# Kernel tuning notes

Hardware: AMD Instinct MI355X
Metric: run time of the kernel (lower is better)

## Reference

```python
import jax, jax.numpy as jnp
import numpy as np

D = 768
H = 12
HD = D // H
EPS = 1e-5

def layer_norm(x, g, b):
    xf = x.astype(jnp.float32)
    mu = jnp.mean(xf, axis=-1, keepdims=True)
    var = jnp.var(xf, axis=-1, keepdims=True)
    return ((xf - mu) * jax.lax.rsqrt(var + EPS) * g + b).astype(x.dtype)

def quick_gelu(x):
    return x * jax.nn.sigmoid(1.702 * x)

def setup_inputs() -> dict:
    key = jax.random.key(0)
    ks = jax.random.split(key, 8)
    L, N = 257, 64
    s = 1.0 / np.sqrt(D)
    return {
        "x": jax.random.normal(ks[0], (L, N, D), dtype=jnp.float32),
        "in_proj_w": jax.random.normal(ks[1], (3 * D, D), dtype=jnp.float32) * s,
        "in_proj_b": jnp.zeros((3 * D,), dtype=jnp.float32),
        "out_proj_w": jax.random.normal(ks[2], (D, D), dtype=jnp.float32) * s,
        "out_proj_b": jnp.zeros((D,), dtype=jnp.float32),
        "ln1_g": jnp.ones((D,), dtype=jnp.float32),
        "ln1_b": jnp.zeros((D,), dtype=jnp.float32),
        "ln2_g": jnp.ones((D,), dtype=jnp.float32),
        "ln2_b": jnp.zeros((D,), dtype=jnp.float32),
        "fc_w": jax.random.normal(ks[3], (D, D), dtype=jnp.float32) * s,
        "fc_b": jnp.zeros((D,), dtype=jnp.float32),
    }

def reference(x, in_proj_w, in_proj_b, out_proj_w, out_proj_b,
              ln1_g, ln1_b, ln2_g, ln2_b, fc_w, fc_b):
    L, N, _ = x.shape
    h = layer_norm(x, ln1_g, ln1_b)                      # [L,N,D]
    qkv = h @ in_proj_w.T + in_proj_b                    # [L,N,3D]
    q, k, v = jnp.split(qkv, 3, axis=-1)
    q = q.reshape(L, N, H, HD)
    k = k.reshape(L, N, H, HD)
    v = v.reshape(L, N, H, HD)
    scale = 1.0 / np.sqrt(HD)
    scores = jnp.einsum('lnhd,mnhd->nhlm', q, k) * scale  # [N,H,L,L]
    weights = jax.nn.softmax(scores, axis=-1)             # per-head attn weights
    attn = jnp.einsum('nhlm,mnhd->lnhd', weights, v).reshape(L, N, D)
    attn_out = attn @ out_proj_w.T + out_proj_b
    x = x + attn_out
    h2 = layer_norm(x, ln2_g, ln2_b)
    x = x + quick_gelu(h2 @ fc_w.T + fc_b)
    return x, weights
```

## Files before the change

### kernel.cpp

```cpp
#include <hip/hip_runtime.h>
#include <cstdint>

#define D_MODEL 768
#define NHEAD 12
#define HDIM 64
#define LSEQ 257
#define NBATCH 64
#define MROWS (LSEQ*NBATCH)

typedef unsigned short u16;
typedef __attribute__((ext_vector_type(8))) short short8;
typedef __attribute__((ext_vector_type(4))) float floatx4;

__device__ __forceinline__ float b2f(u16 u){ return __uint_as_float(((unsigned)u)<<16); }
__device__ __forceinline__ u16 f2bf(float f){
  unsigned x = __float_as_uint(f);
  return (u16)((x + 0x7fffu + ((x>>16)&1u)) >> 16);
}

__device__ __forceinline__ void async16(const u16* g, u16* l) {
  __builtin_amdgcn_global_load_lds(
      (const __attribute__((address_space(1))) unsigned int*)g,
      (__attribute__((address_space(3))) unsigned int*)l, 16, 0, 0);
}

__global__ __launch_bounds__(256) void cvt_bf16(const float* __restrict__ in,
                                                u16* __restrict__ out, int n8)
{
  int i = blockIdx.x*256 + threadIdx.x;
  if (i >= n8) return;
  const float4* p = (const float4*)in + (size_t)i*2;
  float4 a = p[0], b = p[1];
  u16 t[8] = {f2bf(a.x),f2bf(a.y),f2bf(a.z),f2bf(a.w),
              f2bf(b.x),f2bf(b.y),f2bf(b.z),f2bf(b.w)};
  *(uint4*)(out + (size_t)i*8) = *(const uint4*)t;
}

template<typename TIN>
__global__ __launch_bounds__(256) void ln_kernel(const TIN* __restrict__ x,
    const float* __restrict__ g, const float* __restrict__ b,
    u16* __restrict__ out, int rows)
{
  int wv = threadIdx.x >> 6, lane = threadIdx.x & 63;
  int row = blockIdx.x*4 + wv;
  if (row >= rows) return;
  const TIN* xr = x + (size_t)row*D_MODEL;
  float v[12]; float s = 0.f, s2 = 0.f;
#pragma unroll
  for (int i=0;i<12;++i){
    float f;
    if constexpr (sizeof(TIN)==2) f = b2f(((const u16*)xr)[lane + i*64]);
    else                          f = ((const float*)xr)[lane + i*64];
    v[i]=f; s+=f; s2+=f*f;
  }
#pragma unroll
  for (int o=32;o>0;o>>=1){ s += __shfl_xor(s,o,64); s2 += __shfl_xor(s2,o,64); }
  float mu = s*(1.f/768.f);
  float var = fmaxf(s2*(1.f/768.f) - mu*mu, 0.f);
  float rs = rsqrtf(var + 1e-5f);
  u16* orow = out + (size_t)row*D_MODEL;
#pragma unroll
  for (int i=0;i<12;++i){
    int c = lane + i*64;
    orow[c] = f2bf((v[i]-mu)*rs*g[c] + b[c]);
  }
}

#define BM 128
#define BN 128
#define BK 64

template<int EPI>
__global__ __launch_bounds__(256,2) void gemm_bt(
    const u16* __restrict__ A, const u16* __restrict__ B,
    const float* __restrict__ bias, void* __restrict__ Cout,
    const void* __restrict__ resid, int M, int N, int K)
{
  __shared__ u16 sA[BM*BK];
  __shared__ u16 sB[BN*BK];
  const int m0 = blockIdx.y * BM, n0 = blockIdx.x * BN;
  const int tid = threadIdx.x;
  const int lane = tid & 63, w = tid >> 6;
  const int wm = (w>>1)*64, wn = (w&1)*64;
  const int l16 = lane & 15, quad = lane >> 4;
  const int srow = lane >> 3;
  const int scol = ((lane & 7) ^ srow) * 8;
  const u16* gA[4]; const u16* gB[4];
#pragma unroll
  for (int c=0;c<4;++c) {
    int ra = m0 + w*32 + c*8 + srow; if (ra >= M) ra = M-1;
    gA[c] = A + (size_t)ra*K + scol;
    int rb = n0 + w*32 + c*8 + srow;
    gB[c] = B + (size_t)rb*K + scol;
  }
  u16* lA0 = sA + w*32*BK;
  u16* lB0 = sB + w*32*BK;

  floatx4 acc[4][4];
#pragma unroll
  for (int i=0;i<4;++i)
#pragma unroll
    for (int j=0;j<4;++j) acc[i][j] = (floatx4){0.f,0.f,0.f,0.f};

  for (int k0=0;k0<K;k0+=BK) {
#pragma unroll
    for (int c=0;c<4;++c) async16(gA[c] + k0, lA0 + c*8*BK);
#pragma unroll
    for (int c=0;c<4;++c) async16(gB[c] + k0, lB0 + c*8*BK);
    __syncthreads();
#pragma unroll
    for (int ks=0;ks<2;++ks) {
      short8 af[4], bfr[4];
#pragma unroll
      for (int t=0;t<4;++t)
        af[t]  = *(const short8*)(sA + (wm + t*16 + l16)*BK + ((ks*4+quad) ^ (l16&7))*8);
#pragma unroll
      for (int t=0;t<4;++t)
        bfr[t] = *(const short8*)(sB + (wn + t*16 + l16)*BK + ((ks*4+quad) ^ (l16&7))*8);
#pragma unroll
      for (int mt=0;mt<4;++mt)
#pragma unroll
        for (int nt=0;nt<4;++nt)
          acc[mt][nt] = __builtin_amdgcn_mfma_f32_16x16x32_bf16(af[mt], bfr[nt], acc[mt][nt], 0,0,0);
    }
    __syncthreads();
  }

#pragma unroll
  for (int mt=0;mt<4;++mt)
#pragma unroll
    for (int nt=0;nt<4;++nt) {
      int col = n0 + wn + nt*16 + l16;
      if (col >= N) continue;
      float bia = bias[col];
      int rowb = m0 + wm + mt*16 + quad*4;
#pragma unroll
      for (int r=0;r<4;++r) {
        int row = rowb + r;
        if (row >= M) continue;
        float vacc = acc[mt][nt][r] + bia;
        size_t off = (size_t)row*N + col;
        if (EPI==0) {
          ((u16*)Cout)[off] = f2bf(vacc);
        } else if (EPI==1) {
          ((u16*)Cout)[off] = f2bf(((const float*)resid)[off] + vacc);
        } else {
          float gl = vacc / (1.f + __expf(-1.702f*vacc));
          ((float*)Cout)[off] = b2f(((const u16*)resid)[off]) + gl;
        }
      }
    }
}

__global__ __launch_bounds__(256,2) void attn_kernel(
    const u16* __restrict__ qkv, float* __restrict__ wout, u16* __restrict__ attn)
{
  __shared__ __align__(16) u16 smem[29696];
  u16* sQ  = smem;
  u16* sK  = smem + 64*72;
  u16* sP  = smem;
  u16* sVt = smem + 64*296;
  const int p = blockIdx.x;
  const int n = p / NHEAD, h = p % NHEAD;
  const int l0 = blockIdx.y * 64;
  const int tid = threadIdx.x, lane = tid & 63, w = tid >> 6;
  const int l16 = lane & 15, quad = lane >> 4;

  for (int i = tid; i < 64*8; i += 256) {
    int lr = i >> 3, c8 = (i & 7)*8;
    uint4 v = {0u,0u,0u,0u};
    int gl = l0 + lr;
    if (gl < LSEQ) v = *(const uint4*)(qkv + ((size_t)gl*NBATCH + n)*2304 + h*HDIM + c8);
    *(uint4*)(sQ + lr*72 + c8) = v;
  }
  for (int i = tid; i < 272*8; i += 256) {
    int kr = i >> 3, c8 = (i & 7)*8;
    uint4 v = {0u,0u,0u,0u};
    if (kr < LSEQ) v = *(const uint4*)(qkv + ((size_t)kr*NBATCH + n)*2304 + 768 + h*HDIM + c8);
    *(uint4*)(sK + kr*72 + c8) = v;
  }
  __syncthreads();

  floatx4 acc[17];
#pragma unroll
  for (int t=0;t<17;++t) acc[t] = (floatx4){0.f,0.f,0.f,0.f};
#pragma unroll
  for (int ks=0;ks<2;++ks) {
    short8 aq = *(const short8*)(sQ + (w*16 + l16)*72 + ks*32 + quad*8);
#pragma unroll
    for (int nt=0;nt<17;++nt) {
      short8 bk = *(const short8*)(sK + (nt*16 + l16)*72 + ks*32 + quad*8);
      acc[nt] = __builtin_amdgcn_mfma_f32_16x16x32_bf16(aq, bk, acc[nt], 0,0,0);
    }
  }
  __syncthreads();

#pragma unroll
  for (int r=0;r<4;++r) {
    float mx = -3.0e38f;
#pragma unroll
    for (int nt=0;nt<17;++nt) {
      int col = nt*16 + l16;
      float v = (col < LSEQ) ? acc[nt][r]*0.125f : -3.0e38f;
      acc[nt][r] = v;
      mx = fmaxf(mx, v);
    }
#pragma unroll
    for (int o=1;o<16;o<<=1) mx = fmaxf(mx, __shfl_xor(mx,o,64));
    float sum = 0.f;
#pragma unroll
    for (int nt=0;nt<17;++nt) {
      float e = __expf(acc[nt][r]-mx);
      acc[nt][r] = e; sum += e;
    }
#pragma unroll
    for (int o=1;o<16;o<<=1) sum += __shfl_xor(sum,o,64);
    float inv = 1.f/sum;
#pragma unroll
    for (int nt=0;nt<17;++nt) acc[nt][r] *= inv;
  }

  size_t wbase = (size_t)p * LSEQ * LSEQ;
#pragma unroll
  for (int r=0;r<4;++r) {
    int lr = w*16 + quad*4 + r;
    int gl = l0 + lr;
#pragma unroll
    for (int nt=0;nt<17;++nt) {
      int col = nt*16 + l16;
      sP[lr*296 + col] = f2bf(acc[nt][r]);
      if (gl < LSEQ && col < LSEQ) wout[wbase + (size_t)gl*LSEQ + col] = acc[nt][r];
    }
  }
  for (int i = tid; i < 64*16; i += 256) {
    int lr = i >> 4, c = 272 + (i & 15);
    sP[lr*296 + c] = 0;
  }
  __syncthreads();

  floatx4 acc2[4];
#pragma unroll
  for (int t=0;t<4;++t) acc2[t] = (floatx4){0.f,0.f,0.f,0.f};
  for (int c=0;c<2;++c) {
    if (c) __syncthreads();
    int mbase = c*160;
    int msz = c ? 128 : 160;
    for (int ml = tid; ml < msz; ml += 256) {
      int m = mbase + ml;
      if (m < LSEQ) {
        const u16* vr = qkv + ((size_t)m*NBATCH + n)*2304 + 1536 + h*HDIM;
#pragma unroll
        for (int d=0; d<64; ++d) sVt[d*168 + ml] = vr[d];
      } else {
#pragma unroll
        for (int d=0; d<64; ++d) sVt[d*168 + ml] = 0;
      }
    }
    __syncthreads();
    int nks = c ? 4 : 5;
    for (int ksl=0; ksl<nks; ++ksl) {
      short8 ap = *(const short8*)(sP + (w*16 + l16)*296 + mbase + ksl*32 + quad*8);
#pragma unroll
      for (int nt=0;nt<4;++nt) {
        short8 bv = *(const short8*)(sVt + (nt*16 + l16)*168 + ksl*32 + quad*8);
        acc2[nt] = __builtin_amdgcn_mfma_f32_16x16x32_bf16(ap, bv, acc2[nt], 0,0,0);
      }
    }
  }
#pragma unroll
  for (int nt=0;nt<4;++nt)
#pragma unroll
    for (int r=0;r<4;++r) {
      int lr = w*16 + quad*4 + r;
      int gl = l0 + lr;
      if (gl < LSEQ) {
        int d = nt*16 + l16;
        attn[((size_t)gl*NBATCH + n)*768 + h*HDIM + d] = f2bf(acc2[nt][r]);
      }
    }
}

extern "C" void kernel_launch(void* const* d_in, const int* in_sizes, int n_in,
                              void* d_out, int out_size, void* d_ws, size_t ws_size,
                              hipStream_t stream)
{
  (void)in_sizes; (void)n_in; (void)out_size; (void)ws_size;
  const float* x    = (const float*)d_in[0];
  const float* w_in = (const float*)d_in[1];
  const float* b_in = (const float*)d_in[2];
  const float* w_op = (const float*)d_in[3];
  const float* b_op = (const float*)d_in[4];
  const float* g1   = (const float*)d_in[5];
  const float* b1   = (const float*)d_in[6];
  const float* g2   = (const float*)d_in[7];
  const float* b2v  = (const float*)d_in[8];
  const float* wfc  = (const float*)d_in[9];
  const float* bfc  = (const float*)d_in[10];

  float* out_x = (float*)d_out;
  float* out_w = out_x + (size_t)MROWS*D_MODEL;

  char* ws = (char*)d_ws;
  u16* qkv  = (u16*)ws;
  u16* hbuf = (u16*)(ws + (size_t)MROWS*2304*2);
  u16* x2b  = (u16*)(ws + (size_t)MROWS*2304*2 + (size_t)MROWS*768*2);

  u16* w_in_bf = x2b;
  u16* w_op_bf = qkv + (size_t)24*1024*1024;
  u16* w_fc_bf = w_op_bf + 768*768;

  dim3 blk(256);
  cvt_bf16<<<dim3(864), blk, 0, stream>>>(w_in, w_in_bf, 221184);
  ln_kernel<float><<<dim3(MROWS/4), blk, 0, stream>>>(x, g1, b1, hbuf, MROWS);
  gemm_bt<0><<<dim3(18,129), blk, 0, stream>>>(hbuf, w_in_bf, b_in, qkv, nullptr, MROWS, 2304, 768);
  attn_kernel<<<dim3(768,5), blk, 0, stream>>>(qkv, out_w, hbuf);
  cvt_bf16<<<dim3(288), blk, 0, stream>>>(w_op, w_op_bf, 73728);
  cvt_bf16<<<dim3(288), blk, 0, stream>>>(wfc,  w_fc_bf, 73728);
  gemm_bt<1><<<dim3(6,129), blk, 0, stream>>>(hbuf, w_op_bf, b_op, x2b, x, MROWS, 768, 768);
  ln_kernel<u16><<<dim3(MROWS/4), blk, 0, stream>>>(x2b, g2, b2v, qkv, MROWS);
  gemm_bt<2><<<dim3(6,129), blk, 0, stream>>>(qkv, w_fc_bf, bfc, out_x, x2b, MROWS, 768, 768);
}
```

Baseline: 611.4 us.

## Double-buffer GEMM shared-memory tiles to overlap global loads with MFMA

The GEMM main loop now keeps two shared-memory buffers for A and B. It issues the asynchronous global-to-LDS loads for the next K tile before computing on the current one, and uses explicit vmcnt waits with raw barriers in place of __syncthreads. This hides global load latency behind the MFMA work. In exchange, LDS per block doubles to 64KB, which may limit occupancy at two blocks per CU, and correctness depends on the hand-written waitcnt values.

```diff
diff --git a/kernel.cpp b/kernel.cpp
--- a/kernel.cpp
+++ b/kernel.cpp
@@ -76,8 +76,8 @@
     const float* __restrict__ bias, void* __restrict__ Cout,
     const void* __restrict__ resid, int M, int N, int K)
 {
-  __shared__ u16 sA[BM*BK];
-  __shared__ u16 sB[BN*BK];
+  __shared__ u16 sA[2][BM*BK];
+  __shared__ u16 sB[2][BN*BK];
   const int m0 = blockIdx.y * BM, n0 = blockIdx.x * BN;
   const int tid = threadIdx.x;
   const int lane = tid & 63, w = tid >> 6;
@@ -93,8 +93,7 @@
     int rb = n0 + w*32 + c*8 + srow;
     gB[c] = B + (size_t)rb*K + scol;
   }
-  u16* lA0 = sA + w*32*BK;
-  u16* lB0 = sB + w*32*BK;
+  const int lw = w*32*BK;
 
   floatx4 acc[4][4];
 #pragma unroll
@@ -102,35 +101,50 @@
 #pragma unroll
     for (int j=0;j<4;++j) acc[i][j] = (floatx4){0.f,0.f,0.f,0.f};
 
-  for (int k0=0;k0<K;k0+=BK) {
-#pragma unroll
-    for (int c=0;c<4;++c) async16(gA[c] + k0, lA0 + c*8*BK);
-#pragma unroll
-    for (int c=0;c<4;++c) async16(gB[c] + k0, lB0 + c*8*BK);
-    __syncthreads();
+  const int nt = K >> 6;
+#pragma unroll
+  for (int c=0;c<4;++c) async16(gA[c], &sA[0][lw + c*8*BK]);
+#pragma unroll
+  for (int c=0;c<4;++c) async16(gB[c], &sB[0][lw + c*8*BK]);
+
+  for (int t=0; t<nt; ++t) {
+    const int cur = t & 1;
+    if (t+1 < nt) {
+      const int k1 = (t+1)*BK;
+#pragma unroll
+      for (int c=0;c<4;++c) async16(gA[c] + k1, &sA[1-cur][lw + c*8*BK]);
+#pragma unroll
+      for (int c=0;c<4;++c) async16(gB[c] + k1, &sB[1-cur][lw + c*8*BK]);
+      asm volatile("s_waitcnt vmcnt(8)" ::: "memory");
+    } else {
+      asm volatile("s_waitcnt vmcnt(0)" ::: "memory");
+    }
+    __builtin_amdgcn_s_barrier();
+    __builtin_amdgcn_sched_barrier(0);
 #pragma unroll
     for (int ks=0;ks<2;++ks) {
       short8 af[4], bfr[4];
 #pragma unroll
-      for (int t=0;t<4;++t)
-        af[t]  = *(const short8*)(sA + (wm + t*16 + l16)*BK + ((ks*4+quad) ^ (l16&7))*8);
-#pragma unroll
-      for (int t=0;t<4;++t)
-        bfr[t] = *(const short8*)(sB + (wn + t*16 + l16)*BK + ((ks*4+quad) ^ (l16&7))*8);
+      for (int tt=0;tt<4;++tt)
+        af[tt]  = *(const short8*)(&sA[cur][(wm + tt*16 + l16)*BK + ((ks*4+quad) ^ (l16&7))*8]);
+#pragma unroll
+      for (int tt=0;tt<4;++tt)
+        bfr[tt] = *(const short8*)(&sB[cur][(wn + tt*16 + l16)*BK + ((ks*4+quad) ^ (l16&7))*8]);
 #pragma unroll
       for (int mt=0;mt<4;++mt)
 #pragma unroll
-        for (int nt=0;nt<4;++nt)
-          acc[mt][nt] = __builtin_amdgcn_mfma_f32_16x16x32_bf16(af[mt], bfr[nt], acc[mt][nt], 0,0,0);
-    }
-    __syncthreads();
+        for (int ntt=0;ntt<4;++ntt)
+          acc[mt][ntt] = __builtin_amdgcn_mfma_f32_16x16x32_bf16(af[mt], bfr[ntt], acc[mt][ntt], 0,0,0);
+    }
+    __builtin_amdgcn_sched_barrier(0);
+    __builtin_amdgcn_s_barrier();
   }
 
 #pragma unroll
   for (int mt=0;mt<4;++mt)
 #pragma unroll
-    for (int nt=0;nt<4;++nt) {
-      int col = n0 + wn + nt*16 + l16;
+    for (int ntc=0;ntc<4;++ntc) {
+      int col = n0 + wn + ntc*16 + l16;
       if (col >= N) continue;
       float bia = bias[col];
       int rowb = m0 + wm + mt*16 + quad*4;
@@ -138,7 +152,7 @@
       for (int r=0;r<4;++r) {
         int row = rowb + r;
         if (row >= M) continue;
-        float vacc = acc[mt][nt][r] + bia;
+        float vacc = acc[mt][ntc][r] + bia;
         size_t off = (size_t)row*N + col;
         if (EPI==0) {
           ((u16*)Cout)[off] = f2bf(vacc);
```

Result: slower. 694.2 us (+13.5%).
